# Performance work log

Hardware: AMD Instinct MI355X
Metric: run time of the kernel (lower is better)

The kernel has to match this reference:

```python
import jax, jax.numpy as jnp
import numpy as np

EMB = 512       # emb_dim
H = 8           # n_heads
HD = EMB // H   # head_dim = 64
FREQ = 64       # freq_features
PERIOD = 0.1
N = 2048


def setup_inputs() -> dict:
    key = jax.random.key(0)
    ks = jax.random.split(key, 6)
    x = jax.random.normal(ks[0], (1, N, EMB), dtype=jnp.float32)
    v = jax.random.normal(ks[1], (1, N, 3), dtype=jnp.float32)
    vec_map = v / jnp.linalg.norm(v, axis=-1, keepdims=True)  # unit direction vectors
    s_in = 1.0 / np.sqrt(EMB)
    W_qkv = jax.random.normal(ks[2], (EMB, 3 * EMB), dtype=jnp.float32) * s_in
    b_qkv = jnp.zeros((3 * EMB,), dtype=jnp.float32)
    W_bias = jax.random.normal(ks[3], (FREQ, H), dtype=jnp.float32) * (1.0 / np.sqrt(FREQ))
    b_bias = jnp.zeros((H,), dtype=jnp.float32)
    W_out = jax.random.normal(ks[4], (EMB, EMB), dtype=jnp.float32) * s_in
    b_out = jnp.zeros((EMB,), dtype=jnp.float32)
    return {"x": x, "vec_map": vec_map, "W_qkv": W_qkv, "b_qkv": b_qkv,
            "W_bias": W_bias, "b_bias": b_bias, "W_out": W_out, "b_out": b_out}


def reference(x, vec_map, W_qkv, b_qkv, W_bias, b_bias, W_out, b_out):
    batch_dim = x.shape[:-2]
    n = x.shape[-2]
    # QKV projection -> (*, N, H, 3, HD)
    qkv = (x @ W_qkv + b_qkv).reshape(*batch_dim, n, H, 3, HD)
    q, k, v = (qkv[..., 0, :], qkv[..., 1, :], qkv[..., 2, :])
    # attention scores (*, Q, K, H), softmax over the K axis (axis=-2)
    attn = jnp.einsum('...qht,...kht->...qkh', q, k) / np.sqrt(HD)
    attn = jax.nn.softmax(attn, axis=-2)
    # relative bias from pairwise angles between direction vectors
    dot = jnp.einsum('...nc,...mc->...nm', vec_map, vec_map)
    angle = jnp.arccos(jnp.clip(dot, 0.0, 1.0)) / 0.001
    freqs = jnp.linspace(0.0, 1.0, FREQ // 2, dtype=jnp.float32) / PERIOD
    phase = freqs * angle[..., None]                      # (*, N, N, FREQ/2)
    pos = jnp.concatenate((jnp.sin(phase), jnp.cos(phase)), axis=-1)  # (*, N, N, FREQ)
    bias = pos @ W_bias + b_bias                          # (*, N, N, H)
    attn = attn + bias
    # weighted sum of values -> (*, N, EMB)
    y = jnp.einsum('...qkh,...kht->...qht', attn, v).reshape(*batch_dim, n, EMB)
    return y @ W_out + b_out
```

## Files before the change

### kernel.cpp

```cpp
#include <hip/hip_runtime.h>
#include <hip/hip_bf16.h>
#include <math.h>

#define NT 2048
#define EMBD 512
#define NH 8
#define QKV_LD 1536
#define KSPLIT 8

typedef unsigned short u16;
typedef __attribute__((ext_vector_type(8))) short short8;
typedef __attribute__((ext_vector_type(4))) float v4f;

static __device__ __forceinline__ float bf2f(unsigned int u) {
    union { unsigned int i; float f; } c; c.i = u << 16; return c.f;
}
static __device__ __forceinline__ unsigned int f2bf(float x) {
    union { float f; unsigned int u; } c; c.f = x;
    return (c.u + 0x7fffu + ((c.u >> 16) & 1u)) >> 16;
}
static __device__ __forceinline__ unsigned int cvtpk(float lo, float hi) {
    unsigned int r;
    asm("v_cvt_pk_bf16_f32 %0, %1, %2" : "=v"(r) : "v"(lo), "v"(hi));
    return r;
}

__global__ __launch_bounds__(256) void prep(const float* __restrict__ x,
    u16* __restrict__ xh, u16* __restrict__ xl,
    const float* __restrict__ Wqkv, u16* __restrict__ wth, u16* __restrict__ wtl,
    const float* __restrict__ Wout, u16* __restrict__ woth, u16* __restrict__ wotl)
{
    __shared__ float tile[64][65];
    int b = blockIdx.x;
    const int t = threadIdx.x;
    if (b < 1024) {
        int i = (b * 256 + t) << 2;
        float4 v = *(const float4*)(x + i);
        float f[4] = {v.x, v.y, v.z, v.w};
        unsigned int hi[4], lo[4];
#pragma unroll
        for (int j = 0; j < 4; ++j) {
            hi[j] = f2bf(f[j]);
            lo[j] = f2bf(f[j] - bf2f(hi[j]));
        }
        uint2 wh; wh.x = hi[0] | (hi[1] << 16); wh.y = hi[2] | (hi[3] << 16);
        uint2 wl; wl.x = lo[0] | (lo[1] << 16); wl.y = lo[2] | (lo[3] << 16);
        *(uint2*)(xh + i) = wh;
        *(uint2*)(xl + i) = wl;
        return;
    }
    b -= 1024;
    const float* W; u16* th; u16* tl; int ld, bx, by;
    if (b < 192) { W = Wqkv; th = wth;  tl = wtl;  ld = QKV_LD; bx = b % 24; by = b / 24; }
    else { b -= 192; W = Wout; th = woth; tl = wotl; ld = EMBD; bx = b & 7; by = b >> 3; }
    const int n0 = bx << 6, k0 = by << 6;
    const int r = t >> 2, c4 = (t & 3) << 4;
#pragma unroll
    for (int j = 0; j < 4; ++j)
        *(float4*)&tile[r][c4 + (j << 2)] =
            *(const float4*)(W + (size_t)(k0 + r) * ld + n0 + c4 + (j << 2));
    __syncthreads();
    const int n_l = t >> 2;
    u16 vh[16], vl[16];
#pragma unroll
    for (int j = 0; j < 16; ++j) {
        float f = tile[c4 + j][n_l];
        unsigned int h = f2bf(f);
        vh[j] = (u16)h;
        vl[j] = (u16)f2bf(f - bf2f(h));
    }
    u16* dh = th + (size_t)(n0 + n_l) * EMBD + k0 + c4;
    u16* dl = tl + (size_t)(n0 + n_l) * EMBD + k0 + c4;
    *(uint4*)dh       = *(uint4*)&vh[0];
    *(uint4*)(dh + 8) = *(uint4*)&vh[8];
    *(uint4*)dl       = *(uint4*)&vl[0];
    *(uint4*)(dl + 8) = *(uint4*)&vl[8];
}

__global__ __launch_bounds__(256) void gemm_qkv_mfma(const u16* __restrict__ xh,
    const u16* __restrict__ xl, const u16* __restrict__ wth,
    const u16* __restrict__ wtl, const float* __restrict__ bias,
    u16* __restrict__ qkvb)
{
    const int n0 = blockIdx.x << 6, m0 = blockIdx.y << 6;
    const int w = threadIdx.x >> 6, lane = threadIdx.x & 63;
    const int wm = w >> 1, wn = w & 1;
    const int fr = lane & 15, kd = (lane >> 4) << 3;

    const u16* ah0 = xh + (size_t)(m0 + wm * 32 + fr) * EMBD + kd;
    const u16* al0 = xl + (size_t)(m0 + wm * 32 + fr) * EMBD + kd;
    const u16* bh0 = wth + (size_t)(n0 + wn * 32 + fr) * EMBD + kd;
    const u16* bl0 = wtl + (size_t)(n0 + wn * 32 + fr) * EMBD + kd;

    v4f acc[2][2] = {};
    for (int kc = 0; kc < EMBD; kc += 32) {
        short8 a_h[2], a_l[2], b_h[2], b_l[2];
#pragma unroll
        for (int im = 0; im < 2; ++im) {
            a_h[im] = *(const short8*)(ah0 + (size_t)im * 16 * EMBD + kc);
            a_l[im] = *(const short8*)(al0 + (size_t)im * 16 * EMBD + kc);
        }
#pragma unroll
        for (int in = 0; in < 2; ++in) {
            b_h[in] = *(const short8*)(bh0 + (size_t)in * 16 * EMBD + kc);
            b_l[in] = *(const short8*)(bl0 + (size_t)in * 16 * EMBD + kc);
        }
#pragma unroll
        for (int im = 0; im < 2; ++im)
#pragma unroll
            for (int in = 0; in < 2; ++in) {
                acc[im][in] = __builtin_amdgcn_mfma_f32_16x16x32_bf16(a_h[im], b_h[in], acc[im][in], 0, 0, 0);
                acc[im][in] = __builtin_amdgcn_mfma_f32_16x16x32_bf16(a_h[im], b_l[in], acc[im][in], 0, 0, 0);
                acc[im][in] = __builtin_amdgcn_mfma_f32_16x16x32_bf16(a_l[im], b_h[in], acc[im][in], 0, 0, 0);
            }
    }
    const int qr = (lane >> 4) << 2;
#pragma unroll
    for (int im = 0; im < 2; ++im)
#pragma unroll
        for (int in = 0; in < 2; ++in) {
            int n = n0 + wn * 32 + in * 16 + fr;
            float bv = bias[n];
#pragma unroll
            for (int r = 0; r < 4; ++r) {
                int m = m0 + wm * 32 + im * 16 + qr + r;
                qkvb[(size_t)m * QKV_LD + n] = (u16)f2bf(acc[im][in][r] + bv);
            }
        }
}

__global__ __launch_bounds__(256) void transpose_v(const u16* __restrict__ qkvb,
                                                   u16* __restrict__ Vt)
{
    __shared__ u16 tile[64][72];
    const int h = blockIdx.y, k0 = blockIdx.x << 6;
    const int t = threadIdx.x;
    {
        int r = t >> 2, cg = (t & 3) << 4;
        const u16* src = qkvb + (size_t)(k0 + r) * QKV_LD + h * 192 + 128 + cg;
        *(uint4*)&tile[r][cg]     = *(const uint4*)src;
        *(uint4*)&tile[r][cg + 8] = *(const uint4*)(src + 8);
    }
    __syncthreads();
    {
        int c = t >> 2, kg = (t & 3) << 4;
        u16 tmp[16];
#pragma unroll
        for (int j = 0; j < 16; ++j) tmp[j] = tile[kg + j][c];
        u16* dst = Vt + ((size_t)h * 64 + c) * NT + k0 + kg;
        *(uint4*)dst       = *(uint4*)&tmp[0];
        *(uint4*)(dst + 8) = *(uint4*)&tmp[8];
    }
}

__global__ __launch_bounds__(512, 2) void fused_attn(
    const u16* __restrict__ qkvb, const u16* __restrict__ Vt,
    const float* __restrict__ vec, const float* __restrict__ Wb,
    const float* __restrict__ bb, float* __restrict__ zpart,
    float* __restrict__ partsP, float* __restrict__ partsB)
{
    __shared__ float flds[32];
    __shared__ float vql[96];
    __shared__ float ang[32 * 65];
    __shared__ u16 tile[8 * 2056];

    const int bid = blockIdx.x;
    const int zsp = bid & 7;
    const int qt  = bid >> 3;
    const int q0 = qt << 5;
    const int kbase = zsp << 8;

    const int t = threadIdx.x;
    const int w = t >> 6;
    const int lane = t & 63;
    const int fr = lane & 15;
    const int hi4 = lane >> 4;
    const int kd = hi4 << 3;
    const int qr = hi4 << 2;

    if (t < 32) flds[t] = __fdiv_rn(__fdiv_rn((float)t, 31.0f), 0.1f);
    else if (t < 128) vql[t - 32] = vec[q0 * 3 + (t - 32)];

    short8 BS, BC;
#pragma unroll
    for (int j = 0; j < 8; ++j) {
        float ws = (fr < 8) ? Wb[(kd + j) * 8 + fr] : 0.0f;
        float wc = (fr < 8) ? Wb[(32 + kd + j) * 8 + fr] : 0.0f;
        BS[j] = (short)f2bf(ws);
        BC[j] = (short)f2bf(wc);
    }
    const float bbv = (fr < 8) ? bb[fr] : 0.0f;

    short8 aq[2][2];
#pragma unroll
    for (int mb = 0; mb < 2; ++mb)
#pragma unroll
        for (int kk = 0; kk < 2; ++kk)
            aq[mb][kk] = *(const short8*)(qkvb +
                (size_t)(q0 + mb * 16 + fr) * QKV_LD + w * 192 + kk * 32 + kd);

    v4f accP[2][4] = {};
    v4f accB[2][4] = {};
    float zacc[2][4] = {};

    __syncthreads();

    for (int c = 0; c < 4; ++c) {
        const int kc = kbase + (c << 6);
        {
            const int p0 = t << 2;
            const int q = p0 >> 6;
            const int kl = p0 & 63;
            const float a0 = vql[q * 3], a1 = vql[q * 3 + 1], a2 = vql[q * 3 + 2];
            const float* vk = vec + (size_t)(kc + kl) * 3;
#pragma unroll
            for (int j = 0; j < 4; ++j) {
                float c0 = vk[j * 3], c1 = vk[j * 3 + 1], c2 = vk[j * 3 + 2];
                float dot = __fadd_rn(__fadd_rn(__fmul_rn(a0, c0), __fmul_rn(a1, c1)),
                                      __fmul_rn(a2, c2));
                float dotc = fminf(fmaxf(dot, 0.0f), 1.0f);
                ang[q * 65 + kl + j] = __fdiv_rn(acosf(dotc), 0.001f);
            }
        }
        __syncthreads();
#pragma unroll
        for (int gi = 0; gi < 16; ++gi) {
            const int g = w + (gi << 3);
            const int q = g >> 2;
            const int ksub = (g & 3) << 4;
            const float av = ang[q * 65 + ksub + fr];
            float sv[8], cv[8];
#pragma unroll
            for (int j = 0; j < 8; ++j) {
                float ph = __fmul_rn(flds[kd + j], av);
                float rv = ph * 0.15915494309189535f;
                float rf = rv - floorf(rv);
                sv[j] = __builtin_amdgcn_sinf(rf);
                cv[j] = __builtin_amdgcn_cosf(rf);
            }
            union { uint4 u; short8 v; } As, Ac;
            As.u.x = cvtpk(sv[0], sv[1]); As.u.y = cvtpk(sv[2], sv[3]);
            As.u.z = cvtpk(sv[4], sv[5]); As.u.w = cvtpk(sv[6], sv[7]);
            Ac.u.x = cvtpk(cv[0], cv[1]); Ac.u.y = cvtpk(cv[2], cv[3]);
            Ac.u.z = cvtpk(cv[4], cv[5]); Ac.u.w = cvtpk(cv[6], cv[7]);
            v4f cb = {};
            cb = __builtin_amdgcn_mfma_f32_16x16x32_bf16(As.v, BS, cb, 0, 0, 0);
            cb = __builtin_amdgcn_mfma_f32_16x16x32_bf16(Ac.v, BC, cb, 0, 0, 0);
            if (fr < 8) {
                const int kg = (ksub + qr) >> 3;
                uint2 wv;
                wv.x = cvtpk(cb[0] + bbv, cb[1] + bbv);
                wv.y = cvtpk(cb[2] + bbv, cb[3] + bbv);
                *(uint2*)&tile[fr * 2056 + q * 64 + ((kg ^ (q & 7)) << 3) + (qr & 7)] = wv;
            }
        }
        __syncthreads();
        short8 vb[4][2], bk[4][2];
#pragma unroll
        for (int nt = 0; nt < 4; ++nt)
#pragma unroll
            for (int kk = 0; kk < 2; ++kk) {
                vb[nt][kk] = *(const short8*)(Vt +
                    (size_t)(w * 64 + nt * 16 + fr) * NT + kc + kk * 32 + kd);
                bk[nt][kk] = *(const short8*)(qkvb +
                    (size_t)(kc + nt * 16 + fr) * QKV_LD + w * 192 + 64 + kk * 32 + kd);
            }
#pragma unroll
        for (int mb = 0; mb < 2; ++mb) {
            const int q = mb * 16 + fr;
#pragma unroll
            for (int kk = 0; kk < 2; ++kk) {
                short8 ab = *(const short8*)&tile[w * 2056 + q * 64 +
                    (((kk * 4 + hi4) ^ (q & 7)) << 3)];
#pragma unroll
                for (int nt = 0; nt < 4; ++nt)
                    accB[mb][nt] = __builtin_amdgcn_mfma_f32_16x16x32_bf16(ab, vb[nt][kk], accB[mb][nt], 0, 0, 0);
            }
        }
        v4f sacc[2][4] = {};
#pragma unroll
        for (int mb = 0; mb < 2; ++mb)
#pragma unroll
            for (int nt = 0; nt < 4; ++nt) {
                sacc[mb][nt] = __builtin_amdgcn_mfma_f32_16x16x32_bf16(aq[mb][0], bk[nt][0], sacc[mb][nt], 0, 0, 0);
                sacc[mb][nt] = __builtin_amdgcn_mfma_f32_16x16x32_bf16(aq[mb][1], bk[nt][1], sacc[mb][nt], 0, 0, 0);
            }
        unsigned int pk[2][4][2];
#pragma unroll
        for (int mb = 0; mb < 2; ++mb)
#pragma unroll
            for (int nt = 0; nt < 4; ++nt)
#pragma unroll
                for (int r2 = 0; r2 < 2; ++r2) {
                    float e0 = __expf(sacc[mb][nt][2 * r2] * 0.125f);
                    float e1 = __expf(sacc[mb][nt][2 * r2 + 1] * 0.125f);
                    zacc[mb][2 * r2] += e0;
                    zacc[mb][2 * r2 + 1] += e1;
                    pk[mb][nt][r2] = cvtpk(e0, e1);
                }
        __syncthreads();
#pragma unroll
        for (int mb = 0; mb < 2; ++mb)
#pragma unroll
            for (int nt = 0; nt < 4; ++nt) {
                const int kg = (nt << 1) + (fr >> 3);
#pragma unroll
                for (int r = 0; r < 4; ++r) {
                    const int q = mb * 16 + qr + r;
                    tile[w * 2056 + q * 64 + ((kg ^ (q & 7)) << 3) + (fr & 7)] =
                        (u16)(pk[mb][nt][r >> 1] >> ((r & 1) << 4));
                }
            }
        __syncthreads();
#pragma unroll
        for (int mb = 0; mb < 2; ++mb) {
            const int q = mb * 16 + fr;
#pragma unroll
            for (int kk = 0; kk < 2; ++kk) {
                short8 ap = *(const short8*)&tile[w * 2056 + q * 64 +
                    (((kk * 4 + hi4) ^ (q & 7)) << 3)];
#pragma unroll
                for (int nt = 0; nt < 4; ++nt)
                    accP[mb][nt] = __builtin_amdgcn_mfma_f32_16x16x32_bf16(ap, vb[nt][kk], accP[mb][nt], 0, 0, 0);
            }
        }
    }
#pragma unroll
    for (int off = 1; off < 16; off <<= 1)
#pragma unroll
        for (int mb = 0; mb < 2; ++mb)
#pragma unroll
            for (int r = 0; r < 4; ++r)
                zacc[mb][r] += __shfl_xor(zacc[mb][r], off);
    if (fr == 0) {
#pragma unroll
        for (int mb = 0; mb < 2; ++mb)
#pragma unroll
            for (int r = 0; r < 4; ++r)
                zpart[((size_t)zsp * 8 + w) * NT + q0 + mb * 16 + qr + r] = zacc[mb][r];
    }
    float* pP = partsP + (size_t)zsp * NT * EMBD;
    float* pB = partsB + (size_t)zsp * NT * EMBD;
#pragma unroll
    for (int mb = 0; mb < 2; ++mb)
#pragma unroll
        for (int nt = 0; nt < 4; ++nt)
#pragma unroll
            for (int r = 0; r < 4; ++r) {
                const size_t idx = (size_t)(q0 + mb * 16 + qr + r) * EMBD +
                                   (w << 6) + (nt << 4) + fr;
                pP[idx] = accP[mb][nt][r];
                pB[idx] = accB[mb][nt][r];
            }
}

__global__ __launch_bounds__(256) void reduce_y2(const float* __restrict__ partsP,
    const float* __restrict__ partsB, const float* __restrict__ zpart,
    u16* __restrict__ yh, u16* __restrict__ yl)
{
    const int MN = NT * EMBD;
    int i = (blockIdx.x * 256 + threadIdx.x) << 2;
    const int q = i >> 9;
    const int h = (i & 511) >> 6;
    float zs = 0.0f;
#pragma unroll
    for (int z = 0; z < KSPLIT; ++z) zs += zpart[((size_t)z * 8 + h) * NT + q];
    float4 aP = *(const float4*)(partsP + i);
    float4 aB = *(const float4*)(partsB + i);
#pragma unroll
    for (int z = 1; z < KSPLIT; ++z) {
        float4 p = *(const float4*)(partsP + (size_t)z * MN + i);
        float4 b = *(const float4*)(partsB + (size_t)z * MN + i);
        aP.x += p.x; aP.y += p.y; aP.z += p.z; aP.w += p.w;
        aB.x += b.x; aB.y += b.y; aB.z += b.z; aB.w += b.w;
    }
    const float iz = 1.0f / zs;
    float f[4] = {aP.x * iz + aB.x, aP.y * iz + aB.y,
                  aP.z * iz + aB.z, aP.w * iz + aB.w};
    unsigned int hi[4], lo[4];
#pragma unroll
    for (int j = 0; j < 4; ++j) {
        hi[j] = f2bf(f[j]);
        lo[j] = f2bf(f[j] - bf2f(hi[j]));
    }
    uint2 wh; wh.x = hi[0] | (hi[1] << 16); wh.y = hi[2] | (hi[3] << 16);
    uint2 wl; wl.x = lo[0] | (lo[1] << 16); wl.y = lo[2] | (lo[3] << 16);
    *(uint2*)(yh + i) = wh;
    *(uint2*)(yl + i) = wl;
}

__global__ __launch_bounds__(256) void gemm_out_mfma(const u16* __restrict__ yh,
    const u16* __restrict__ yl, const u16* __restrict__ wh,
    const u16* __restrict__ wl, const float* __restrict__ bias,
    float* __restrict__ out)
{
    const int n0 = blockIdx.x << 6, m0 = blockIdx.y << 6;
    const int w = threadIdx.x >> 6, lane = threadIdx.x & 63;
    const int wm = w >> 1, wn = w & 1;
    const int fr = lane & 15, kd = (lane >> 4) << 3;

    const u16* ah0 = yh + (size_t)(m0 + wm * 32 + fr) * EMBD + kd;
    const u16* al0 = yl + (size_t)(m0 + wm * 32 + fr) * EMBD + kd;
    const u16* bh0 = wh + (size_t)(n0 + wn * 32 + fr) * EMBD + kd;
    const u16* bl0 = wl + (size_t)(n0 + wn * 32 + fr) * EMBD + kd;

    v4f acc[2][2] = {};
    for (int kc = 0; kc < EMBD; kc += 32) {
        short8 a_h[2], a_l[2], b_h[2], b_l[2];
#pragma unroll
        for (int im = 0; im < 2; ++im) {
            a_h[im] = *(const short8*)(ah0 + (size_t)im * 16 * EMBD + kc);
            a_l[im] = *(const short8*)(al0 + (size_t)im * 16 * EMBD + kc);
        }
#pragma unroll
        for (int in = 0; in < 2; ++in) {
            b_h[in] = *(const short8*)(bh0 + (size_t)in * 16 * EMBD + kc);
            b_l[in] = *(const short8*)(bl0 + (size_t)in * 16 * EMBD + kc);
        }
#pragma unroll
        for (int im = 0; im < 2; ++im)
#pragma unroll
            for (int in = 0; in < 2; ++in) {
                acc[im][in] = __builtin_amdgcn_mfma_f32_16x16x32_bf16(a_h[im], b_h[in], acc[im][in], 0, 0, 0);
                acc[im][in] = __builtin_amdgcn_mfma_f32_16x16x32_bf16(a_h[im], b_l[in], acc[im][in], 0, 0, 0);
                acc[im][in] = __builtin_amdgcn_mfma_f32_16x16x32_bf16(a_l[im], b_h[in], acc[im][in], 0, 0, 0);
            }
    }
    const int qr = (lane >> 4) << 2;
#pragma unroll
    for (int im = 0; im < 2; ++im)
#pragma unroll
        for (int in = 0; in < 2; ++in) {
            int n = n0 + wn * 32 + in * 16 + fr;
            float bv = bias[n];
#pragma unroll
            for (int r = 0; r < 4; ++r) {
                int m = m0 + wm * 32 + im * 16 + qr + r;
                out[(size_t)m * EMBD + n] = acc[im][in][r] + bv;
            }
        }
}

extern "C" void kernel_launch(void* const* d_in, const int* in_sizes, int n_in,
                              void* d_out, int out_size, void* d_ws, size_t ws_size,
                              hipStream_t stream)
{
    const float* x    = (const float*)d_in[0];
    const float* vec  = (const float*)d_in[1];
    const float* Wqkv = (const float*)d_in[2];
    const float* bqkv = (const float*)d_in[3];
    const float* Wb   = (const float*)d_in[4];
    const float* bb   = (const float*)d_in[5];
    const float* Wout = (const float*)d_in[6];
    const float* bout = (const float*)d_in[7];
    float* out = (float*)d_out;

    char* ws = (char*)d_ws;
    u16*   qkvb   = (u16*)(ws);
    u16*   Vt     = (u16*)(ws + 6291456);
    float* zpart  = (float*)(ws + 8388608);
    float* partsP = (float*)(ws + 8912896);
    float* partsB = (float*)(ws + 42467328);
    u16*   yh     = (u16*)(ws + 76021760);
    u16*   yl     = (u16*)(ws + 78118912);
    u16*   xh     = (u16*)(ws + 80216064);
    u16*   xl     = (u16*)(ws + 82313216);
    u16*   wth    = (u16*)(ws + 84410368);
    u16*   wtl    = (u16*)(ws + 85983232);
    u16*   woth   = (u16*)(ws + 87556096);
    u16*   wotl   = (u16*)(ws + 88080384);

    prep<<<1280, 256, 0, stream>>>(x, xh, xl, Wqkv, wth, wtl, Wout, woth, wotl);
    gemm_qkv_mfma<<<dim3(24, 32), 256, 0, stream>>>(xh, xl, wth, wtl, bqkv, qkvb);
    transpose_v<<<dim3(32, 8), 256, 0, stream>>>(qkvb, Vt);
    fused_attn<<<64 * KSPLIT, 512, 0, stream>>>(qkvb, Vt, vec, Wb, bb,
                                                zpart, partsP, partsB);
    reduce_y2<<<1024, 256, 0, stream>>>(partsP, partsB, zpart, yh, yl);
    gemm_out_mfma<<<dim3(8, 32), 256, 0, stream>>>(yh, yl, woth, wotl, bout, out);
}
```

Before: 255.3 us.

## Split fused attention kernel into separate bias-V and softmax-PV kernels

The single fused attention kernel is split into two launches. bias_v computes the angle-based bias, projects it through W_bias and multiplies it by V. attn_pv computes QK scores, exp and P·V. The aim is to cut register pressure and barrier count per kernel so bias_v can run with higher occupancy, and attn_pv drops its __syncthreads because each wave only touches its own LDS slice. The cost is an extra launch, V being read twice from global memory, and the loss of overlap between the two halves inside one block.

```diff
diff --git a/kernel.cpp b/kernel.cpp
--- a/kernel.cpp
+++ b/kernel.cpp
@@ -153,15 +153,10 @@
     }
 }
 
-__global__ __launch_bounds__(512, 2) void fused_attn(
+__global__ __launch_bounds__(512, 2) void attn_pv(
     const u16* __restrict__ qkvb, const u16* __restrict__ Vt,
-    const float* __restrict__ vec, const float* __restrict__ Wb,
-    const float* __restrict__ bb, float* __restrict__ zpart,
-    float* __restrict__ partsP, float* __restrict__ partsB)
-{
-    __shared__ float flds[32];
-    __shared__ float vql[96];
-    __shared__ float ang[32 * 65];
+    float* __restrict__ zpart, float* __restrict__ partsP)
+{
     __shared__ u16 tile[8 * 2056];
 
     const int bid = blockIdx.x;
@@ -178,6 +173,124 @@
     const int kd = hi4 << 3;
     const int qr = hi4 << 2;
 
+    short8 aq[2][2];
+#pragma unroll
+    for (int mb = 0; mb < 2; ++mb)
+#pragma unroll
+        for (int kk = 0; kk < 2; ++kk)
+            aq[mb][kk] = *(const short8*)(qkvb +
+                (size_t)(q0 + mb * 16 + fr) * QKV_LD + w * 192 + kk * 32 + kd);
+
+    v4f accP[2][4] = {};
+    float zacc[2][4] = {};
+
+    for (int c = 0; c < 4; ++c) {
+        const int kc = kbase + (c << 6);
+        short8 vb[4][2], bk[4][2];
+#pragma unroll
+        for (int nt = 0; nt < 4; ++nt)
+#pragma unroll
+            for (int kk = 0; kk < 2; ++kk) {
+                vb[nt][kk] = *(const short8*)(Vt +
+                    (size_t)(w * 64 + nt * 16 + fr) * NT + kc + kk * 32 + kd);
+                bk[nt][kk] = *(const short8*)(qkvb +
+                    (size_t)(kc + nt * 16 + fr) * QKV_LD + w * 192 + 64 + kk * 32 + kd);
+            }
+        v4f sacc[2][4] = {};
+#pragma unroll
+        for (int mb = 0; mb < 2; ++mb)
+#pragma unroll
+            for (int nt = 0; nt < 4; ++nt) {
+                sacc[mb][nt] = __builtin_amdgcn_mfma_f32_16x16x32_bf16(aq[mb][0], bk[nt][0], sacc[mb][nt], 0, 0, 0);
+                sacc[mb][nt] = __builtin_amdgcn_mfma_f32_16x16x32_bf16(aq[mb][1], bk[nt][1], sacc[mb][nt], 0, 0, 0);
+            }
+        unsigned int pk[2][4][2];
+#pragma unroll
+        for (int mb = 0; mb < 2; ++mb)
+#pragma unroll
+            for (int nt = 0; nt < 4; ++nt)
+#pragma unroll
+                for (int r2 = 0; r2 < 2; ++r2) {
+                    float e0 = __expf(sacc[mb][nt][2 * r2] * 0.125f);
+                    float e1 = __expf(sacc[mb][nt][2 * r2 + 1] * 0.125f);
+                    zacc[mb][2 * r2] += e0;
+                    zacc[mb][2 * r2 + 1] += e1;
+                    pk[mb][nt][r2] = cvtpk(e0, e1);
+                }
+#pragma unroll
+        for (int mb = 0; mb < 2; ++mb)
+#pragma unroll
+            for (int nt = 0; nt < 4; ++nt) {
+                const int kg = (nt << 1) + (fr >> 3);
+#pragma unroll
+                for (int r = 0; r < 4; ++r) {
+                    const int q = mb * 16 + qr + r;
+                    tile[w * 2056 + q * 64 + ((kg ^ (q & 7)) << 3) + (fr & 7)] =
+                        (u16)(pk[mb][nt][r >> 1] >> ((r & 1) << 4));
+                }
+            }
+#pragma unroll
+        for (int mb = 0; mb < 2; ++mb) {
+            const int q = mb * 16 + fr;
+#pragma unroll
+            for (int kk = 0; kk < 2; ++kk) {
+                short8 ap = *(const short8*)&tile[w * 2056 + q * 64 +
+                    (((kk * 4 + hi4) ^ (q & 7)) << 3)];
+#pragma unroll
+                for (int nt = 0; nt < 4; ++nt)
+                    accP[mb][nt] = __builtin_amdgcn_mfma_f32_16x16x32_bf16(ap, vb[nt][kk], accP[mb][nt], 0, 0, 0);
+            }
+        }
+    }
+#pragma unroll
+    for (int off = 1; off < 16; off <<= 1)
+#pragma unroll
+        for (int mb = 0; mb < 2; ++mb)
+#pragma unroll
+            for (int r = 0; r < 4; ++r)
+                zacc[mb][r] += __shfl_xor(zacc[mb][r], off);
+    if (fr == 0) {
+#pragma unroll
+        for (int mb = 0; mb < 2; ++mb)
+#pragma unroll
+            for (int r = 0; r < 4; ++r)
+                zpart[((size_t)zsp * 8 + w) * NT + q0 + mb * 16 + qr + r] = zacc[mb][r];
+    }
+    float* pP = partsP + (size_t)zsp * NT * EMBD;
+#pragma unroll
+    for (int mb = 0; mb < 2; ++mb)
+#pragma unroll
+        for (int nt = 0; nt < 4; ++nt)
+#pragma unroll
+            for (int r = 0; r < 4; ++r)
+                pP[(size_t)(q0 + mb * 16 + qr + r) * EMBD +
+                   (w << 6) + (nt << 4) + fr] = accP[mb][nt][r];
+}
+
+__global__ __launch_bounds__(512, 4) void bias_v(
+    const u16* __restrict__ Vt, const float* __restrict__ vec,
+    const float* __restrict__ Wb, const float* __restrict__ bb,
+    float* __restrict__ partsB)
+{
+    __shared__ float flds[32];
+    __shared__ float vql[96];
+    __shared__ float ang[32 * 65];
+    __shared__ u16 tile[8 * 2056];
+
+    const int bid = blockIdx.x;
+    const int zsp = bid & 7;
+    const int qt  = bid >> 3;
+    const int q0 = qt << 5;
+    const int kbase = zsp << 8;
+
+    const int t = threadIdx.x;
+    const int w = t >> 6;
+    const int lane = t & 63;
+    const int fr = lane & 15;
+    const int hi4 = lane >> 4;
+    const int kd = hi4 << 3;
+    const int qr = hi4 << 2;
+
     if (t < 32) flds[t] = __fdiv_rn(__fdiv_rn((float)t, 31.0f), 0.1f);
     else if (t < 128) vql[t - 32] = vec[q0 * 3 + (t - 32)];
 
@@ -191,17 +304,7 @@
     }
     const float bbv = (fr < 8) ? bb[fr] : 0.0f;
 
-    short8 aq[2][2];
-#pragma unroll
-    for (int mb = 0; mb < 2; ++mb)
-#pragma unroll
-        for (int kk = 0; kk < 2; ++kk)
-            aq[mb][kk] = *(const short8*)(qkvb +
-                (size_t)(q0 + mb * 16 + fr) * QKV_LD + w * 192 + kk * 32 + kd);
-
-    v4f accP[2][4] = {};
     v4f accB[2][4] = {};
-    float zacc[2][4] = {};
 
     __syncthreads();
 
@@ -255,103 +358,31 @@
             }
         }
         __syncthreads();
-        short8 vb[4][2], bk[4][2];
+#pragma unroll
+        for (int kk = 0; kk < 2; ++kk) {
+            const int q0l = 0 * 16 + fr, q1l = 1 * 16 + fr;
+            short8 ab0 = *(const short8*)&tile[w * 2056 + q0l * 64 +
+                (((kk * 4 + hi4) ^ (q0l & 7)) << 3)];
+            short8 ab1 = *(const short8*)&tile[w * 2056 + q1l * 64 +
+                (((kk * 4 + hi4) ^ (q1l & 7)) << 3)];
+#pragma unroll
+            for (int nt = 0; nt < 4; ++nt) {
+                short8 vbx = *(const short8*)(Vt +
+                    (size_t)(w * 64 + nt * 16 + fr) * NT + kc + kk * 32 + kd);
+                accB[0][nt] = __builtin_amdgcn_mfma_f32_16x16x32_bf16(ab0, vbx, accB[0][nt], 0, 0, 0);
+                accB[1][nt] = __builtin_amdgcn_mfma_f32_16x16x32_bf16(ab1, vbx, accB[1][nt], 0, 0, 0);
+            }
+        }
+    }
+    float* pB = partsB + (size_t)zsp * NT * EMBD;
+#pragma unroll
+    for (int mb = 0; mb < 2; ++mb)
 #pragma unroll
         for (int nt = 0; nt < 4; ++nt)
 #pragma unroll
-            for (int kk = 0; kk < 2; ++kk) {
-                vb[nt][kk] = *(const short8*)(Vt +
-                    (size_t)(w * 64 + nt * 16 + fr) * NT + kc + kk * 32 + kd);
-                bk[nt][kk] = *(const short8*)(qkvb +
-                    (size_t)(kc + nt * 16 + fr) * QKV_LD + w * 192 + 64 + kk * 32 + kd);
-            }
-#pragma unroll
-        for (int mb = 0; mb < 2; ++mb) {
-            const int q = mb * 16 + fr;
-#pragma unroll
-            for (int kk = 0; kk < 2; ++kk) {
-                short8 ab = *(const short8*)&tile[w * 2056 + q * 64 +
-                    (((kk * 4 + hi4) ^ (q & 7)) << 3)];
-#pragma unroll
-                for (int nt = 0; nt < 4; ++nt)
-                    accB[mb][nt] = __builtin_amdgcn_mfma_f32_16x16x32_bf16(ab, vb[nt][kk], accB[mb][nt], 0, 0, 0);
-            }
-        }
-        v4f sacc[2][4] = {};
-#pragma unroll
-        for (int mb = 0; mb < 2; ++mb)
-#pragma unroll
-            for (int nt = 0; nt < 4; ++nt) {
-                sacc[mb][nt] = __builtin_amdgcn_mfma_f32_16x16x32_bf16(aq[mb][0], bk[nt][0], sacc[mb][nt], 0, 0, 0);
-                sacc[mb][nt] = __builtin_amdgcn_mfma_f32_16x16x32_bf16(aq[mb][1], bk[nt][1], sacc[mb][nt], 0, 0, 0);
-            }
-        unsigned int pk[2][4][2];
-#pragma unroll
-        for (int mb = 0; mb < 2; ++mb)
-#pragma unroll
-            for (int nt = 0; nt < 4; ++nt)
-#pragma unroll
-                for (int r2 = 0; r2 < 2; ++r2) {
-                    float e0 = __expf(sacc[mb][nt][2 * r2] * 0.125f);
-                    float e1 = __expf(sacc[mb][nt][2 * r2 + 1] * 0.125f);
-                    zacc[mb][2 * r2] += e0;
-                    zacc[mb][2 * r2 + 1] += e1;
-                    pk[mb][nt][r2] = cvtpk(e0, e1);
-                }
-        __syncthreads();
-#pragma unroll
-        for (int mb = 0; mb < 2; ++mb)
-#pragma unroll
-            for (int nt = 0; nt < 4; ++nt) {
-                const int kg = (nt << 1) + (fr >> 3);
-#pragma unroll
-                for (int r = 0; r < 4; ++r) {
-                    const int q = mb * 16 + qr + r;
-                    tile[w * 2056 + q * 64 + ((kg ^ (q & 7)) << 3) + (fr & 7)] =
-                        (u16)(pk[mb][nt][r >> 1] >> ((r & 1) << 4));
-                }
-            }
-        __syncthreads();
-#pragma unroll
-        for (int mb = 0; mb < 2; ++mb) {
-            const int q = mb * 16 + fr;
-#pragma unroll
-            for (int kk = 0; kk < 2; ++kk) {
-                short8 ap = *(const short8*)&tile[w * 2056 + q * 64 +
-                    (((kk * 4 + hi4) ^ (q & 7)) << 3)];
-#pragma unroll
-                for (int nt = 0; nt < 4; ++nt)
-                    accP[mb][nt] = __builtin_amdgcn_mfma_f32_16x16x32_bf16(ap, vb[nt][kk], accP[mb][nt], 0, 0, 0);
-            }
-        }
-    }
-#pragma unroll
-    for (int off = 1; off < 16; off <<= 1)
-#pragma unroll
-        for (int mb = 0; mb < 2; ++mb)
-#pragma unroll
             for (int r = 0; r < 4; ++r)
-                zacc[mb][r] += __shfl_xor(zacc[mb][r], off);
-    if (fr == 0) {
-#pragma unroll
-        for (int mb = 0; mb < 2; ++mb)
-#pragma unroll
-            for (int r = 0; r < 4; ++r)
-                zpart[((size_t)zsp * 8 + w) * NT + q0 + mb * 16 + qr + r] = zacc[mb][r];
-    }
-    float* pP = partsP + (size_t)zsp * NT * EMBD;
-    float* pB = partsB + (size_t)zsp * NT * EMBD;
-#pragma unroll
-    for (int mb = 0; mb < 2; ++mb)
-#pragma unroll
-        for (int nt = 0; nt < 4; ++nt)
-#pragma unroll
-            for (int r = 0; r < 4; ++r) {
-                const size_t idx = (size_t)(q0 + mb * 16 + qr + r) * EMBD +
-                                   (w << 6) + (nt << 4) + fr;
-                pP[idx] = accP[mb][nt][r];
-                pB[idx] = accB[mb][nt][r];
-            }
+                pB[(size_t)(q0 + mb * 16 + qr + r) * EMBD +
+                   (w << 6) + (nt << 4) + fr] = accB[mb][nt][r];
 }
 
 __global__ __launch_bounds__(256) void reduce_y2(const float* __restrict__ partsP,
@@ -473,8 +504,8 @@
     prep<<<1280, 256, 0, stream>>>(x, xh, xl, Wqkv, wth, wtl, Wout, woth, wotl);
     gemm_qkv_mfma<<<dim3(24, 32), 256, 0, stream>>>(xh, xl, wth, wtl, bqkv, qkvb);
     transpose_v<<<dim3(32, 8), 256, 0, stream>>>(qkvb, Vt);
-    fused_attn<<<64 * KSPLIT, 512, 0, stream>>>(qkvb, Vt, vec, Wb, bb,
-                                                zpart, partsP, partsB);
+    bias_v<<<64 * KSPLIT, 512, 0, stream>>>(Vt, vec, Wb, bb, partsB);
+    attn_pv<<<64 * KSPLIT, 512, 0, stream>>>(qkvb, Vt, zpart, partsP);
     reduce_y2<<<1024, 256, 0, stream>>>(partsP, partsB, zpart, yh, yl);
     gemm_out_mfma<<<dim3(8, 32), 256, 0, stream>>>(yh, yl, woth, wotl, bout, out);
 }
```

Result: faster. 245.2 us (-3.9%).
